# Kernel optimization log

Measured on AMD Instinct MI355X. Metric: run time of the kernel, lower is better.

Reference implementation:

```python
import jax, jax.numpy as jnp
import numpy as np

B, S, D, H = 4, 2048, 1024, 16
HD = D // H  # head_dim = 64


def setup_inputs() -> dict:
    key = jax.random.key(0)
    ks = jax.random.split(key, 6)
    scale = 1.0 / np.sqrt(D)
    x = jax.random.normal(ks[0], (B, S, D), dtype=jnp.float32)
    mask = jax.random.bernoulli(ks[1], 0.9, (B, S, S))  # bool, True = keep
    wq = jax.random.normal(ks[2], (D, D), dtype=jnp.float32) * scale
    wk = jax.random.normal(ks[3], (D, D), dtype=jnp.float32) * scale
    wv = jax.random.normal(ks[4], (D, D), dtype=jnp.float32) * scale
    wo = jax.random.normal(ks[5], (D, D), dtype=jnp.float32) * scale
    return {"x": x, "mask": mask, "wq": wq, "wk": wk, "wv": wv, "wo": wo}


def reference(x, mask, wq, wk, wv, wo):
    bsz, seqlen, dim = x.shape
    # nn.Linear applies x @ W.T; weights here stored as [out, in]
    xq = (x @ wq.T).reshape(bsz, seqlen, H, HD)
    xk = (x @ wk.T).reshape(bsz, seqlen, H, HD)
    xv = (x @ wv.T).reshape(bsz, seqlen, H, HD)
    # scores: [B, H, S, S]
    scores = jnp.einsum("bqhd,bkhd->bhqk", xq, xk) / np.sqrt(HD).astype(np.float32)
    # additive mask: ~mask * -1e9, broadcast over heads
    neg = jnp.where(mask[:, None, :, :], 0.0, -1e9).astype(scores.dtype)
    scores = scores + neg
    scores = jax.nn.softmax(scores.astype(jnp.float32), axis=-1).astype(xq.dtype)
    # multiplicative re-mask after softmax (as in the original)
    scores = scores * mask[:, None, :, :].astype(scores.dtype)
    out = jnp.einsum("bhqk,bkhd->bqhd", scores, xv).reshape(bsz, seqlen, dim)
    return out @ wo.T
```

## Files before the change

### kernel.cpp

```cpp
#include <hip/hip_runtime.h>
#include <hip/hip_bf16.h>

#define S_LEN 2048
#define DIM   1024
#define NHEAD 16
#define HDIM  64
#define QSCALE 0.18033688f

typedef __attribute__((ext_vector_type(8))) short bfrag;
typedef __attribute__((ext_vector_type(4))) float f32x4;
typedef __attribute__((ext_vector_type(16))) float f32x16;
typedef __attribute__((ext_vector_type(4))) unsigned int u32x4;

#define MFMA(a,b,c)   __builtin_amdgcn_mfma_f32_16x16x32_bf16((a),(b),(c),0,0,0)
#define MFMA32(a,b,c) __builtin_amdgcn_mfma_f32_32x32x16_bf16((a),(b),(c),0,0,0)

__device__ __forceinline__ unsigned short f2bf(float x) {
  __hip_bfloat16 h = __float2bfloat16(x);
  return *reinterpret_cast<unsigned short*>(&h);
}

__device__ __forceinline__ unsigned int pk2bf(float a, float b) {
  float2 f2; f2.x = a; f2.y = b;
  __hip_bfloat162 b2 = __float22bfloat162_rn(f2);
  return *reinterpret_cast<unsigned int*>(&b2);
}

__device__ __forceinline__ void gll16(const unsigned short* g, unsigned short* l) {
  __builtin_amdgcn_global_load_lds(
      (const __attribute__((address_space(1))) unsigned int*)g,
      (__attribute__((address_space(3))) unsigned int*)l, 16, 0, 0);
}

__global__ void probe(const unsigned int* __restrict__ x,
                      const unsigned int* __restrict__ mask,
                      int* __restrict__ flags) {
  const int lane = threadIdx.x;
  int insane = 0;
  for (int i = lane; i < 512; i += 64) {
    unsigned int w = x[i];
    unsigned int e = (w >> 7) & 0xFFu;
    bool sane = (e >= 90u && e <= 160u) || ((w & 0x7FFFu) == 0u);
    insane += sane ? 0 : 1;
  }
  bool all01 = true, allu8 = true, allf32 = true, allbf = true;
  for (int i = lane; i < 1024; i += 64) {
    unsigned int w = mask[i];
    all01  &= (w <= 1u);
    allu8  &= ((w & 0xFEFEFEFEu) == 0u);
    allf32 &= (w == 0u || w == 0x3F800000u);
    unsigned int lo = w & 0xFFFFu, hi = w >> 16;
    allbf  &= (lo == 0u || lo == 0x3F80u) && (hi == 0u || hi == 0x3F80u);
  }
#pragma unroll
  for (int off = 1; off < 64; off <<= 1) insane += __shfl_xor(insane, off, 64);
  const unsigned long long full = ~0ull;
  const bool g01  = __ballot(all01)  == full;
  const bool gu8  = __ballot(allu8)  == full;
  const bool gf32 = __ballot(allf32) == full;
  const bool gbf  = __ballot(allbf)  == full;
  if (lane == 0) {
    flags[0] = (insane > 128) ? 1 : 0;
    flags[1] = g01 ? 1 : (gu8 ? 0 : (gf32 ? 2 : (gbf ? 3 : 0)));
  }
}

__device__ __forceinline__ bool mask_at(const void* mk, int mode, size_t idx) {
  switch (mode) {
    case 0:  return ((const unsigned char*)mk)[idx]  != 0;
    case 1:  return ((const int*)mk)[idx]            != 0;
    case 2:  return ((const unsigned int*)mk)[idx]   != 0u;
    default: return ((const unsigned short*)mk)[idx] != 0;
  }
}

__global__ __launch_bounds__(256) void cvt_all(
    const void* __restrict__ x,  const void* __restrict__ wq,
    const void* __restrict__ wk, const void* __restrict__ wv,
    const void* __restrict__ wo,
    unsigned short* __restrict__ xb,  unsigned short* __restrict__ wqb,
    unsigned short* __restrict__ wkb, unsigned short* __restrict__ wvb,
    unsigned short* __restrict__ wob, const int* __restrict__ flags) {
  const int bx = blockIdx.x;
  const void* src; unsigned short* dst; int i;
  if (bx < 4096) { src = x; dst = xb; i = bx * 256 + threadIdx.x; }
  else {
    const int r = (bx - 4096) >> 9, off = (bx - 4096) & 511;
    src = r == 0 ? wq : r == 1 ? wk : r == 2 ? wv : wo;
    dst = r == 0 ? wqb : r == 1 ? wkb : r == 2 ? wvb : wob;
    i = off * 256 + threadIdx.x;
  }
  if (flags[0]) {
    const float* p = (const float*)src + (size_t)i * 8;
    float4 a = *reinterpret_cast<const float4*>(p);
    float4 b = *reinterpret_cast<const float4*>(p + 4);
    unsigned int d0 = pk2bf(a.x, a.y), d1 = pk2bf(a.z, a.w);
    unsigned int d2 = pk2bf(b.x, b.y), d3 = pk2bf(b.z, b.w);
    uint4 o; o.x = d0; o.y = d1; o.z = d2; o.w = d3;
    *reinterpret_cast<uint4*>(dst + (size_t)i * 8) = o;
  } else {
    *reinterpret_cast<bfrag*>(dst + (size_t)i * 8) =
        reinterpret_cast<const bfrag*>(src)[i];
  }
}

__global__ __launch_bounds__(256) void bitmask(const void* __restrict__ mk,
                                               const int* __restrict__ flags,
                                               unsigned long long* __restrict__ mb) {
  size_t gid = (size_t)blockIdx.x * 256 + threadIdx.x;
  bool v = mask_at(mk, flags[1], gid);
  unsigned long long w = __ballot(v);
  if ((threadIdx.x & 63) == 0) {
    const size_t bb = gid >> 22;
    const size_t q  = (gid >> 11) & 2047;
    const size_t wd = (gid >> 6) & 31;
    mb[(bb * 32 + wd) * 2048 + q] = w;
  }
}

__global__ __launch_bounds__(256) void gemm128(const unsigned short* __restrict__ A,
                                               const unsigned short* __restrict__ Bt,
                                               void* __restrict__ C,
                                               const int* __restrict__ flags,
                                               int aHsplit, int cMode) {
  __shared__ unsigned short As[128 * 32];
  __shared__ unsigned short Bs[128 * 32];
  const int t = threadIdx.x, lane = t & 63, wave = t >> 6;
  const int r16 = lane & 15, quad = lane >> 4;
  const int n0 = blockIdx.x * 128, m0 = blockIdx.y * 128;
  const int wm = (wave >> 1) * 64, wn = (wave & 1) * 64;
  const int arow = t >> 2, aseg = (t & 3) * 8;

  f32x4 acc[4][4];
#pragma unroll
  for (int i = 0; i < 4; ++i)
#pragma unroll
    for (int j = 0; j < 4; ++j) acc[i][j] = (f32x4){0.f, 0.f, 0.f, 0.f};

  for (int k0 = 0; k0 < 1024; k0 += 32) {
    __syncthreads();
#pragma unroll
    for (int rr = 0; rr < 2; ++rr) {
      const int m = m0 + rr * 64 + arow;
      const int k = k0 + aseg;
      const unsigned short* ga;
      if (aHsplit) ga = A + ((size_t)(((m >> 11) << 4) + (k >> 6)) * 2048 + (m & 2047)) * 64 + (k & 63);
      else         ga = A + (size_t)m * 1024 + k;
      gll16(ga, As + rr * 2048 + wave * 512);
      const unsigned short* gb = Bt + (size_t)(n0 + rr * 64 + arow) * 1024 + k0 + aseg;
      gll16(gb, Bs + rr * 2048 + wave * 512);
    }
    __syncthreads();

    bfrag af[4], bf[4];
#pragma unroll
    for (int i = 0; i < 4; ++i)
      af[i] = *reinterpret_cast<const bfrag*>(&As[(wm + i * 16 + r16) * 32 + quad * 8]);
#pragma unroll
    for (int j = 0; j < 4; ++j)
      bf[j] = *reinterpret_cast<const bfrag*>(&Bs[(wn + j * 16 + r16) * 32 + quad * 8]);
#pragma unroll
    for (int i = 0; i < 4; ++i)
#pragma unroll
      for (int j = 0; j < 4; ++j)
        acc[i][j] = MFMA(af[i], bf[j], acc[i][j]);
  }

  const int oF = (cMode == 2) ? flags[0] : 0;
#pragma unroll
  for (int i = 0; i < 4; ++i)
#pragma unroll
    for (int j = 0; j < 4; ++j)
#pragma unroll
      for (int r = 0; r < 4; ++r) {
        const int m = m0 + wm + i * 16 + quad * 4 + r;
        const int n = n0 + wn + j * 16 + r16;
        const float v = acc[i][j][r];
        if (cMode == 3) {
          const int region = n >> 10, nn = n & 1023;
          const float vv = (region == 0) ? v * QSCALE : v;
          const size_t idx = (size_t)region * 8388608 +
              ((size_t)((m >> 11) * NHEAD + (nn >> 6)) * 2048 + (m & 2047)) * 64 + (nn & 63);
          ((unsigned short*)C)[idx] = f2bf(vv);
        } else if (cMode == 1) {
          const size_t idx = ((size_t)((m >> 11) * NHEAD + (n >> 6)) * 2048 + (m & 2047)) * 64 + (n & 63);
          ((unsigned short*)C)[idx] = f2bf(v);
        } else {
          const size_t idx = (size_t)m * 1024 + n;
          if (oF) ((float*)C)[idx] = v;
          else    ((unsigned short*)C)[idx] = f2bf(v);
        }
      }
}

__global__ __launch_bounds__(256) void transposeV(const unsigned short* __restrict__ xvH,
                                                  unsigned short* __restrict__ xvT) {
  __shared__ unsigned short Ts[64 * 80];
  const int t = threadIdx.x;
  const int s0 = blockIdx.x * 64, bh = blockIdx.y;
  const int sr = t >> 3, seg = (t & 7) * 8;
#pragma unroll
  for (int rr = 0; rr < 2; ++rr) {
    const int s = rr * 32 + sr;
    bfrag v = *reinterpret_cast<const bfrag*>(xvH + ((size_t)bh * 2048 + s0 + s) * 64 + seg);
#pragma unroll
    for (int j = 0; j < 8; ++j) Ts[(seg + j) * 80 + s] = (unsigned short)v[j];
  }
  __syncthreads();
#pragma unroll
  for (int rr = 0; rr < 2; ++rr) {
    const int d = rr * 32 + sr;
    bfrag o = *reinterpret_cast<const bfrag*>(&Ts[d * 80 + seg]);
    *reinterpret_cast<bfrag*>(xvT + ((size_t)bh * 64 + d) * 2048 + s0 + seg) = o;
  }
}

#if defined(__has_builtin)
#if __has_builtin(__builtin_amdgcn_permlane32_swap)
#define HAVE_PL32_SWAP 1
#endif
#endif
#ifndef HAVE_PL32_SWAP
#define HAVE_PL32_SWAP 0
#endif

__global__ __launch_bounds__(256) void fattn(const unsigned short* __restrict__ qH,
                                             const unsigned short* __restrict__ kH,
                                             const unsigned short* __restrict__ vT,
                                             const unsigned long long* __restrict__ mbT,
                                             unsigned short* __restrict__ oH) {
  __shared__ unsigned short Ks[2][64 * 64];
  __shared__ unsigned short Vs[2][64 * 64];
  const int t = threadIdx.x, lane = t & 63, wave = t >> 6;
  const int l31 = lane & 31, hi = lane >> 5;
  const int bid = blockIdx.x;
  const int bh = bid & 63, qidx = bid >> 6;
  const int b = bh >> 4;
  const int qw = qidx * 128 + wave * 32;
  const size_t hbase = (size_t)bh * S_LEN;
  const int kgr = l31 & 7;

  bfrag qf[4];
#pragma unroll
  for (int s = 0; s < 4; ++s)
    qf[s] = *reinterpret_cast<const bfrag*>(
        qH + (hbase + qw + l31) * 64 + s * 16 + hi * 8);

  f32x16 o0, o1;
#pragma unroll
  for (int r = 0; r < 16; ++r) { o0[r] = 0.f; o1[r] = 0.f; }
  float ls[4] = {0.f, 0.f, 0.f, 0.f};

  const int srow = lane >> 3;
  const int sg   = (lane & 7) ^ srow;

  auto stage = [&](int buf, int kb) {
#pragma unroll
    for (int rr = 0; rr < 2; ++rr) {
      const int row = rr * 32 + wave * 8 + srow;
      gll16(kH + (hbase + kb + row) * 64 + sg * 8, &Ks[buf][rr * 2048 + wave * 512]);
      gll16(vT + ((size_t)bh * 64 + row) * 2048 + kb + sg * 8, &Vs[buf][rr * 2048 + wave * 512]);
    }
  };

  stage(0, 0);
  int cur = 0;
  const unsigned long long* mcol = mbT + (size_t)b * 32 * S_LEN + (qw + l31);
  unsigned long long wcur = mcol[0];

  for (int kb = 0; kb < S_LEN; kb += 64) {
    __syncthreads();
    const bool more = (kb + 64 < S_LEN);
    if (more) stage(cur ^ 1, kb + 64);
    const unsigned long long wnext =
        more ? mcol[(size_t)((kb >> 6) + 1) * S_LEN] : 0ull;

    const unsigned int wlo = (unsigned int)(wcur >> (4 * hi));
    const unsigned int whi = (unsigned int)(wcur >> (32 + 4 * hi));

#pragma unroll
    for (int c = 0; c < 2; ++c) {
      f32x16 z;
#pragma unroll
      for (int r = 0; r < 16; ++r) z[r] = 0.f;
      __builtin_amdgcn_s_setprio(1);
#pragma unroll
      for (int s = 0; s < 4; ++s) {
        const int gr = (2 * s + hi) ^ kgr;
        bfrag kf = *reinterpret_cast<const bfrag*>(
            &Ks[cur][(c * 32 + l31) * 64 + gr * 8]);
        z = MFMA32(kf, qf[s], z);
      }
      __builtin_amdgcn_s_setprio(0);
      const unsigned int wm = c ? whi : wlo;

#pragma unroll
      for (int s2 = 0; s2 < 2; ++s2) {
        float e[8];
#pragma unroll
        for (int j = 0; j < 8; ++j) {
          const int r = 8 * s2 + j;
          const int bitp = (r & 3) + 8 * (r >> 2);
          float ev = __builtin_amdgcn_exp2f(z[r]);
          ev = (wm & (1u << bitp)) ? ev : 0.f;
          e[j] = ev;
          ls[r & 3] += ev;
        }
        const unsigned int pwa = pk2bf(e[0], e[1]);
        const unsigned int pwb = pk2bf(e[2], e[3]);
        const unsigned int pwc = pk2bf(e[4], e[5]);
        const unsigned int pwd = pk2bf(e[6], e[7]);
        u32x4 uu;
#if HAVE_PL32_SWAP
        auto r02 = __builtin_amdgcn_permlane32_swap(pwa, pwc, false, false);
        auto r13 = __builtin_amdgcn_permlane32_swap(pwb, pwd, false, false);
        uu.x = r02[0];
        uu.y = r13[0];
        uu.z = r02[1];
        uu.w = r13[1];
#else
        const unsigned int t0 = __shfl_xor(pwa, 32, 64);
        const unsigned int t1 = __shfl_xor(pwb, 32, 64);
        const unsigned int t2 = __shfl_xor(pwc, 32, 64);
        const unsigned int t3 = __shfl_xor(pwd, 32, 64);
        uu.x = hi ? t2 : pwa;
        uu.y = hi ? t3 : pwb;
        uu.z = hi ? pwc : t0;
        uu.w = hi ? pwd : t1;
#endif
        const bfrag pf = __builtin_bit_cast(bfrag, uu);
        const int s = 2 * c + s2;
        const int gv = (2 * s + hi) ^ kgr;
        bfrag v0 = *reinterpret_cast<const bfrag*>(&Vs[cur][l31 * 64 + gv * 8]);
        bfrag v1 = *reinterpret_cast<const bfrag*>(&Vs[cur][(32 + l31) * 64 + gv * 8]);
        __builtin_amdgcn_s_setprio(1);
        o0 = MFMA32(pf, v0, o0);
        o1 = MFMA32(pf, v1, o1);
        __builtin_amdgcn_s_setprio(0);
      }
    }
    wcur = wnext;
    cur ^= 1;
  }

  float lsum = (ls[0] + ls[1]) + (ls[2] + ls[3]);
  lsum += __shfl_xor(lsum, 32, 64);
  const float inv = 1.f / fmaxf(lsum, 1e-30f);
#pragma unroll
  for (int r = 0; r < 16; ++r) {
    const int qr = (r & 3) + 8 * (r >> 2) + 4 * hi;
    const float sc = __shfl(inv, qr, 64);
    unsigned short* op = oH + (hbase + qw + qr) * 64 + l31;
    op[0]  = f2bf(o0[r] * sc);
    op[32] = f2bf(o1[r] * sc);
  }
}

template<bool F32>
__device__ __forceinline__ bfrag load8(const void* base, size_t idx) {
  if constexpr (F32) {
    const float* p = (const float*)base + idx;
    float4 u = *reinterpret_cast<const float4*>(p);
    float4 v = *reinterpret_cast<const float4*>(p + 4);
    bfrag r;
    r[0]=(short)f2bf(u.x); r[1]=(short)f2bf(u.y); r[2]=(short)f2bf(u.z); r[3]=(short)f2bf(u.w);
    r[4]=(short)f2bf(v.x); r[5]=(short)f2bf(v.y); r[6]=(short)f2bf(v.z); r[7]=(short)f2bf(v.w);
    return r;
  } else {
    return *reinterpret_cast<const bfrag*>((const unsigned short*)base + idx);
  }
}

template<bool AF32, bool BF32>
__device__ __forceinline__ void gemm_body(const void* __restrict__ A, const void* __restrict__ Bt,
                                          void* __restrict__ C, int N, int K, bool outF32) {
  const int lane = threadIdx.x & 63, wave = threadIdx.x >> 6;
  const int r16 = lane & 15, quad = lane >> 4;
  const int m0 = (blockIdx.y * 4 + wave) * 16, n0 = blockIdx.x * 64;
  f32x4 acc[4];
#pragma unroll
  for (int i = 0; i < 4; ++i) acc[i] = (f32x4){0.f,0.f,0.f,0.f};
  const size_t aoff = (size_t)(m0 + r16) * K + quad * 8;
  const size_t boff = (size_t)(n0 + r16) * K + quad * 8;
  for (int k0 = 0; k0 < K; k0 += 32) {
    bfrag a = load8<AF32>(A, aoff + k0);
#pragma unroll
    for (int tt = 0; tt < 4; ++tt) {
      bfrag bb = load8<BF32>(Bt, boff + (size_t)tt * 16 * K + k0);
      acc[tt] = MFMA(a, bb, acc[tt]);
    }
  }
#pragma unroll
  for (int tt = 0; tt < 4; ++tt)
#pragma unroll
    for (int r = 0; r < 4; ++r) {
      const size_t ci = (size_t)(m0 + quad * 4 + r) * N + n0 + tt * 16 + r16;
      if (outF32) ((float*)C)[ci] = acc[tt][r];
      else        ((unsigned short*)C)[ci] = f2bf(acc[tt][r]);
    }
}

__global__ __launch_bounds__(256) void gemm_bt(const void* A, const void* Bt, void* C,
                                               int N, int K, const int* flags,
                                               int aFollows, int outFollows) {
  const int f = flags[0];
  const bool aF = (aFollows != 0) && (f != 0);
  const bool oF = (outFollows != 0) && (f != 0);
  if (f) { if (aF) gemm_body<true, true>(A, Bt, C, N, K, oF);
           else    gemm_body<false, true>(A, Bt, C, N, K, oF); }
  else     gemm_body<false, false>(A, Bt, C, N, K, oF);
}

__global__ __launch_bounds__(64) void fattn_r2(const unsigned short* __restrict__ xq,
                                               const unsigned short* __restrict__ xk,
                                               const unsigned short* __restrict__ xv,
                                               const void* __restrict__ mk,
                                               const int* __restrict__ flags,
                                               unsigned short* __restrict__ xo) {
  __shared__ unsigned short smemP[16 * 32];
  const int lane = threadIdx.x, r16 = lane & 15, quad = lane >> 4;
  const int q0 = blockIdx.x * 16, h = blockIdx.y, b = blockIdx.z;
  const int mmode = flags[1];
  const size_t base = (size_t)b * S_LEN * DIM + (size_t)h * HDIM;
  const size_t mbase = (size_t)b * S_LEN * S_LEN;
  bfrag aq0 = *reinterpret_cast<const bfrag*>(xq + base + (size_t)(q0 + r16) * DIM + quad * 8);
  bfrag aq1 = *reinterpret_cast<const bfrag*>(xq + base + (size_t)(q0 + r16) * DIM + 32 + quad * 8);
  f32x4 o[4];
#pragma unroll
  for (int i = 0; i < 4; ++i) o[i] = (f32x4){0.f,0.f,0.f,0.f};
  float m_r[4] = {-1e30f,-1e30f,-1e30f,-1e30f}, l_r[4] = {0.f,0.f,0.f,0.f};
  for (int kb = 0; kb < S_LEN; kb += 32) {
    const unsigned short* k0p = xk + base + (size_t)(kb + r16) * DIM + quad * 8;
    const unsigned short* k1p = k0p + (size_t)16 * DIM;
    f32x4 s0 = (f32x4){0.f,0.f,0.f,0.f}, s1 = (f32x4){0.f,0.f,0.f,0.f};
    s0 = MFMA(aq0, *reinterpret_cast<const bfrag*>(k0p), s0);
    s0 = MFMA(aq1, *reinterpret_cast<const bfrag*>(k0p + 32), s0);
    s1 = MFMA(aq0, *reinterpret_cast<const bfrag*>(k1p), s1);
    s1 = MFMA(aq1, *reinterpret_cast<const bfrag*>(k1p + 32), s1);
    float l0[4], l1[4], tmax[4];
#pragma unroll
    for (int r = 0; r < 4; ++r) {
      const size_t mrow = mbase + (size_t)(q0 + quad * 4 + r) * S_LEN + kb;
      l0[r] = mask_at(mk, mmode, mrow + r16) ? s0[r] * 0.125f : -1e30f;
      l1[r] = mask_at(mk, mmode, mrow + 16 + r16) ? s1[r] * 0.125f : -1e30f;
      tmax[r] = fmaxf(l0[r], l1[r]);
    }
#pragma unroll
    for (int off = 1; off < 16; off <<= 1)
#pragma unroll
      for (int r = 0; r < 4; ++r) tmax[r] = fmaxf(tmax[r], __shfl_xor(tmax[r], off, 64));
    float p0[4], p1[4], rsum[4];
#pragma unroll
    for (int r = 0; r < 4; ++r) {
      const float mnew = fmaxf(m_r[r], tmax[r]);
      const float alpha = __expf(m_r[r] - mnew);
      m_r[r] = mnew;
      p0[r] = (l0[r] <= -1e29f) ? 0.f : __expf(l0[r] - mnew);
      p1[r] = (l1[r] <= -1e29f) ? 0.f : __expf(l1[r] - mnew);
      rsum[r] = p0[r] + p1[r];
      l_r[r] *= alpha;
#pragma unroll
      for (int tt = 0; tt < 4; ++tt) o[tt][r] *= alpha;
    }
#pragma unroll
    for (int off = 1; off < 16; off <<= 1)
#pragma unroll
      for (int r = 0; r < 4; ++r) rsum[r] += __shfl_xor(rsum[r], off, 64);
#pragma unroll
    for (int r = 0; r < 4; ++r) l_r[r] += rsum[r];
#pragma unroll
    for (int r = 0; r < 4; ++r) {
      smemP[(quad * 4 + r) * 32 + r16] = f2bf(p0[r]);
      smemP[(quad * 4 + r) * 32 + 16 + r16] = f2bf(p1[r]);
    }
    __syncthreads();
    bfrag apf = *reinterpret_cast<const bfrag*>(&smemP[r16 * 32 + quad * 8]);
    const unsigned short* vbase = xv + base + (size_t)(kb + quad * 8) * DIM + r16;
#pragma unroll
    for (int tt = 0; tt < 4; ++tt) {
      bfrag bv;
#pragma unroll
      for (int j = 0; j < 8; ++j) bv[j] = (short)vbase[(size_t)j * DIM + tt * 16];
      o[tt] = MFMA(apf, bv, o[tt]);
    }
    __syncthreads();
  }
#pragma unroll
  for (int tt = 0; tt < 4; ++tt)
#pragma unroll
    for (int r = 0; r < 4; ++r)
      xo[base + (size_t)(q0 + quad * 4 + r) * DIM + tt * 16 + r16] = f2bf(o[tt][r] / l_r[r]);
}

extern "C" void kernel_launch(void* const* d_in, const int* in_sizes, int n_in,
                              void* d_out, int out_size, void* d_ws, size_t ws_size,
                              hipStream_t stream) {
  const void* x  = d_in[0];
  const void* mk = d_in[1];
  const void* wq = d_in[2];
  const void* wk = d_in[3];
  const void* wv = d_in[4];
  const void* wo = d_in[5];

  const size_t MiB = 1048576;
  const size_t NEED = 4096 + 90 * MiB;

  if (ws_size >= NEED) {
    char* p = (char*)d_ws;
    int* flags = (int*)p;                       p += 4096;
    unsigned short* xb  = (unsigned short*)p;   p += 16 * MiB;
    unsigned short* wqb = (unsigned short*)p;   p += 2 * MiB;
    unsigned short* wkb = (unsigned short*)p;   p += 2 * MiB;
    unsigned short* wvb = (unsigned short*)p;   p += 2 * MiB;
    unsigned short* wob = (unsigned short*)p;   p += 2 * MiB;
    unsigned long long* mb = (unsigned long long*)p; p += 2 * MiB;
    unsigned short* xqH = (unsigned short*)p;   p += 16 * MiB;
    unsigned short* xkH = (unsigned short*)p;   p += 16 * MiB;
    unsigned short* xvH = (unsigned short*)p;   p += 16 * MiB;
    unsigned short* xvT = (unsigned short*)p;   p += 16 * MiB;
    unsigned short* xoH = xvH;

    probe<<<1, 64, 0, stream>>>((const unsigned int*)x, (const unsigned int*)mk, flags);
    cvt_all<<<6144, 256, 0, stream>>>(x, wq, wk, wv, wo, xb, wqb, wkb, wvb, wob, flags);
    bitmask<<<65536, 256, 0, stream>>>(mk, flags, mb);

    gemm128<<<dim3(24, 64), 256, 0, stream>>>(xb, wqb, xqH, flags, 0, 3);
    transposeV<<<dim3(32, 64), 256, 0, stream>>>(xvH, xvT);
    fattn<<<dim3(1024), 256, 0, stream>>>(xqH, xkH, xvT, mb, xoH);
    gemm128<<<dim3(8, 64), 256, 0, stream>>>(xoH, wob, d_out, flags, 1, 2);
  } else {
    int* flags = (int*)d_ws;
    unsigned short* xq = (unsigned short*)((char*)d_ws + 256);
    unsigned short* xk = xq + (size_t)8388608;
    unsigned short* xv = xk + (size_t)8388608;
    unsigned short* xo = xv + (size_t)8388608;
    probe<<<1, 64, 0, stream>>>((const unsigned int*)x, (const unsigned int*)mk, flags);
    dim3 gg(16, 128);
    gemm_bt<<<gg, 256, 0, stream>>>(x, wq, xq, 1024, 1024, flags, 1, 0);
    gemm_bt<<<gg, 256, 0, stream>>>(x, wk, xk, 1024, 1024, flags, 1, 0);
    gemm_bt<<<gg, 256, 0, stream>>>(x, wv, xv, 1024, 1024, flags, 1, 0);
    fattn_r2<<<dim3(128, NHEAD, 4), 64, 0, stream>>>(xq, xk, xv, mk, flags, xo);
    gemm_bt<<<gg, 256, 0, stream>>>(xo, wo, d_out, 1024, 1024, flags, 0, 1);
  }
}
```

Measured before the change: 426.9 us.

## Widen GEMM K-tile with swizzled LDS, remap GEMM blocks, double attention key block

The GEMM now stages a 64-wide K slice per iteration instead of 32. It uses an XOR-swizzled LDS layout to avoid bank conflicts and runs two MFMA sub-steps per barrier. Its workgroup IDs are remapped in groups of eight for better L2 locality. The flash-attention kernel now processes 128 keys per iteration instead of 64, with a wider swizzled V tile and two mask words per step, which halves barrier and prefetch overhead. In exchange, LDS per block doubles (64 KB in attention), which may lower occupancy and latency hiding.

Measured after the change: 404.4 us. 1.06x faster.

```diff
diff --git a/kernel.cpp b/kernel.cpp
--- a/kernel.cpp
+++ b/kernel.cpp
@@ -123,13 +123,21 @@
                                                void* __restrict__ C,
                                                const int* __restrict__ flags,
                                                int aHsplit, int cMode) {
-  __shared__ unsigned short As[128 * 32];
-  __shared__ unsigned short Bs[128 * 32];
+  __shared__ unsigned short As[128 * 64];
+  __shared__ unsigned short Bs[128 * 64];
   const int t = threadIdx.x, lane = t & 63, wave = t >> 6;
   const int r16 = lane & 15, quad = lane >> 4;
-  const int n0 = blockIdx.x * 128, m0 = blockIdx.y * 128;
+
+  const int nwgx = gridDim.x;
+  const int nwg  = nwgx * gridDim.y;
+  const int orig = blockIdx.y * nwgx + blockIdx.x;
+  const int cpx  = nwg >> 3;
+  const int swz  = (orig & 7) * cpx + (orig >> 3);
+  const int n0 = (swz % nwgx) * 128, m0 = (swz / nwgx) * 128;
+
   const int wm = (wave >> 1) * 64, wn = (wave & 1) * 64;
-  const int arow = t >> 2, aseg = (t & 3) * 8;
+  const int srow = t >> 3;
+  const int sgr  = (t & 7) ^ (srow & 7);
 
   f32x4 acc[4][4];
 #pragma unroll
@@ -137,33 +145,39 @@
 #pragma unroll
     for (int j = 0; j < 4; ++j) acc[i][j] = (f32x4){0.f, 0.f, 0.f, 0.f};
 
-  for (int k0 = 0; k0 < 1024; k0 += 32) {
+  for (int k0 = 0; k0 < 1024; k0 += 64) {
     __syncthreads();
 #pragma unroll
-    for (int rr = 0; rr < 2; ++rr) {
-      const int m = m0 + rr * 64 + arow;
-      const int k = k0 + aseg;
+    for (int rr = 0; rr < 4; ++rr) {
+      const int row = rr * 32 + srow;
+      const int m = m0 + row;
+      const int k = k0 + sgr * 8;
       const unsigned short* ga;
       if (aHsplit) ga = A + ((size_t)(((m >> 11) << 4) + (k >> 6)) * 2048 + (m & 2047)) * 64 + (k & 63);
       else         ga = A + (size_t)m * 1024 + k;
       gll16(ga, As + rr * 2048 + wave * 512);
-      const unsigned short* gb = Bt + (size_t)(n0 + rr * 64 + arow) * 1024 + k0 + aseg;
+      const unsigned short* gb = Bt + (size_t)(n0 + row) * 1024 + k;
       gll16(gb, Bs + rr * 2048 + wave * 512);
     }
     __syncthreads();
 
-    bfrag af[4], bf[4];
-#pragma unroll
-    for (int i = 0; i < 4; ++i)
-      af[i] = *reinterpret_cast<const bfrag*>(&As[(wm + i * 16 + r16) * 32 + quad * 8]);
-#pragma unroll
-    for (int j = 0; j < 4; ++j)
-      bf[j] = *reinterpret_cast<const bfrag*>(&Bs[(wn + j * 16 + r16) * 32 + quad * 8]);
-#pragma unroll
-    for (int i = 0; i < 4; ++i)
+#pragma unroll
+    for (int kk = 0; kk < 2; ++kk) {
+      bfrag af[4], bf[4];
+#pragma unroll
+      for (int i = 0; i < 4; ++i)
+        af[i] = *reinterpret_cast<const bfrag*>(
+            &As[(wm + i * 16 + r16) * 64 + (((kk * 4 + quad) ^ (r16 & 7)) * 8)]);
 #pragma unroll
       for (int j = 0; j < 4; ++j)
-        acc[i][j] = MFMA(af[i], bf[j], acc[i][j]);
+        bf[j] = *reinterpret_cast<const bfrag*>(
+            &Bs[(wn + j * 16 + r16) * 64 + (((kk * 4 + quad) ^ (r16 & 7)) * 8)]);
+#pragma unroll
+      for (int i = 0; i < 4; ++i)
+#pragma unroll
+        for (int j = 0; j < 4; ++j)
+          acc[i][j] = MFMA(af[i], bf[j], acc[i][j]);
+    }
   }
 
   const int oF = (cMode == 2) ? flags[0] : 0;
@@ -229,8 +243,8 @@
                                              const unsigned short* __restrict__ vT,
                                              const unsigned long long* __restrict__ mbT,
                                              unsigned short* __restrict__ oH) {
-  __shared__ unsigned short Ks[2][64 * 64];
-  __shared__ unsigned short Vs[2][64 * 64];
+  __shared__ unsigned short Ks[2][128 * 64];
+  __shared__ unsigned short Vs[2][64 * 128];
   const int t = threadIdx.x, lane = t & 63, wave = t >> 6;
   const int l31 = lane & 31, hi = lane >> 5;
   const int bid = blockIdx.x;
@@ -251,35 +265,43 @@
   for (int r = 0; r < 16; ++r) { o0[r] = 0.f; o1[r] = 0.f; }
   float ls[4] = {0.f, 0.f, 0.f, 0.f};
 
-  const int srow = lane >> 3;
-  const int sg   = (lane & 7) ^ srow;
+  const int ksrow = lane >> 3;
+  const int ksg   = (lane & 7) ^ ksrow;
+  const int vsrow = lane >> 4;
+  const int vswz  = (wave * 4 + vsrow) & 7;
+  const int vsg   = (lane & 15) ^ vswz;
 
   auto stage = [&](int buf, int kb) {
 #pragma unroll
-    for (int rr = 0; rr < 2; ++rr) {
-      const int row = rr * 32 + wave * 8 + srow;
-      gll16(kH + (hbase + kb + row) * 64 + sg * 8, &Ks[buf][rr * 2048 + wave * 512]);
-      gll16(vT + ((size_t)bh * 64 + row) * 2048 + kb + sg * 8, &Vs[buf][rr * 2048 + wave * 512]);
+    for (int rr = 0; rr < 4; ++rr) {
+      const int krow = rr * 32 + wave * 8 + ksrow;
+      gll16(kH + (hbase + kb + krow) * 64 + ksg * 8, &Ks[buf][rr * 2048 + wave * 512]);
+      const int vrow = rr * 16 + wave * 4 + vsrow;
+      gll16(vT + ((size_t)bh * 64 + vrow) * 2048 + kb + vsg * 8, &Vs[buf][rr * 2048 + wave * 512]);
     }
   };
 
   stage(0, 0);
   int cur = 0;
   const unsigned long long* mcol = mbT + (size_t)b * 32 * S_LEN + (qw + l31);
-  unsigned long long wcur = mcol[0];
-
-  for (int kb = 0; kb < S_LEN; kb += 64) {
+  unsigned long long wc0 = mcol[0];
+  unsigned long long wc1 = mcol[S_LEN];
+
+  for (int kb = 0; kb < S_LEN; kb += 128) {
     __syncthreads();
-    const bool more = (kb + 64 < S_LEN);
-    if (more) stage(cur ^ 1, kb + 64);
-    const unsigned long long wnext =
-        more ? mcol[(size_t)((kb >> 6) + 1) * S_LEN] : 0ull;
-
-    const unsigned int wlo = (unsigned int)(wcur >> (4 * hi));
-    const unsigned int whi = (unsigned int)(wcur >> (32 + 4 * hi));
-
-#pragma unroll
-    for (int c = 0; c < 2; ++c) {
+    const bool more = (kb + 128 < S_LEN);
+    if (more) stage(cur ^ 1, kb + 128);
+    const int wi = kb >> 6;
+    const unsigned long long wn0 = more ? mcol[(size_t)(wi + 2) * S_LEN] : 0ull;
+    const unsigned long long wn1 = more ? mcol[(size_t)(wi + 3) * S_LEN] : 0ull;
+
+    const unsigned int h0lo = (unsigned int)(wc0 >> (4 * hi));
+    const unsigned int h0hi = (unsigned int)(wc0 >> (32 + 4 * hi));
+    const unsigned int h1lo = (unsigned int)(wc1 >> (4 * hi));
+    const unsigned int h1hi = (unsigned int)(wc1 >> (32 + 4 * hi));
+
+#pragma unroll
+    for (int c = 0; c < 4; ++c) {
       f32x16 z;
 #pragma unroll
       for (int r = 0; r < 16; ++r) z[r] = 0.f;
@@ -292,7 +314,8 @@
         z = MFMA32(kf, qf[s], z);
       }
       __builtin_amdgcn_s_setprio(0);
-      const unsigned int wm = c ? whi : wlo;
+      const unsigned int wm = (c == 0) ? h0lo : (c == 1) ? h0hi
+                            : (c == 2) ? h1lo : h1hi;
 
 #pragma unroll
       for (int s2 = 0; s2 < 2; ++s2) {
@@ -331,15 +354,15 @@
         const bfrag pf = __builtin_bit_cast(bfrag, uu);
         const int s = 2 * c + s2;
         const int gv = (2 * s + hi) ^ kgr;
-        bfrag v0 = *reinterpret_cast<const bfrag*>(&Vs[cur][l31 * 64 + gv * 8]);
-        bfrag v1 = *reinterpret_cast<const bfrag*>(&Vs[cur][(32 + l31) * 64 + gv * 8]);
+        bfrag v0 = *reinterpret_cast<const bfrag*>(&Vs[cur][l31 * 128 + gv * 8]);
+        bfrag v1 = *reinterpret_cast<const bfrag*>(&Vs[cur][(32 + l31) * 128 + gv * 8]);
         __builtin_amdgcn_s_setprio(1);
         o0 = MFMA32(pf, v0, o0);
         o1 = MFMA32(pf, v1, o1);
         __builtin_amdgcn_s_setprio(0);
       }
     }
-    wcur = wnext;
+    wc0 = wn0; wc1 = wn1;
     cur ^= 1;
   }
 
```
